# Kernel tuning notes

Hardware: AMD Instinct MI355X
Metric: run time of the kernel (lower is better)

## Reference

```python
import jax, jax.numpy as jnp
import numpy as np
from itertools import combinations_with_replacement

B, T, F, L, POLY_ORDER = 16, 2048, 128, 16, 3


def _hilbert_filter(N):
    # Matches pytorch_hilbert: H[0]=0, H[1:N//2]=2, H[N//2]=0 (even N)
    h = np.zeros(N, dtype=np.float32)
    if N % 2 == 0:
        h[1:N // 2] = 2.0
    else:
        h[1:(N + 1) // 2] = 2.0
    return jnp.asarray(h)


def hilbert(sig, axis=1):
    N = sig.shape[axis]
    Xf = jnp.fft.fft(sig, axis=axis)
    shape = [1] * sig.ndim
    shape[axis] = N
    return jnp.fft.ifft(Xf * _hilbert_filter(N).reshape(shape), axis=axis)


def _combo_indices(latent, poly_order):
    # static index arrays, grouped by degree n
    return [np.array(list(combinations_with_replacement(range(latent), n)), dtype=np.int32)
            for n in range(1, poly_order + 1)]


def compute_library(z, poly_order):
    # z: [B, T, L] -> theta: [B, T, library_dim]
    feats = []
    for combos in _combo_indices(z.shape[-1], poly_order):
        zc = z[..., combos]            # [B, T, ncomb, n]
        feats.append(jnp.prod(zc, axis=-1))  # [B, T, ncomb]
    analytic = hilbert(z, axis=1)
    feats.append(z)
    feats.append(jnp.abs(analytic))    # extract_real_component
    feats.append(jnp.angle(analytic))  # extract_imaginary_component
    return jnp.concatenate(feats, axis=-1)


def setup_inputs() -> dict:
    key = jax.random.key(0)
    ks = jax.random.split(key, 7)
    lib_dim = L + 2 * L + sum(len(c) for c in _combo_indices(L, POLY_ORDER))
    s_enc = 1.0 / np.sqrt(F)
    s_dec = 1.0 / np.sqrt(L)
    s_sin = 1.0 / np.sqrt(lib_dim)
    return {
        "x": jax.random.normal(ks[0], (B, T, F), dtype=jnp.float32),
        "W_enc": jax.random.uniform(ks[1], (L, F), jnp.float32, -s_enc, s_enc),
        "b_enc": jax.random.uniform(ks[2], (L,), jnp.float32, -s_enc, s_enc),
        "W_dec": jax.random.uniform(ks[3], (F, L), jnp.float32, -s_dec, s_dec),
        "b_dec": jax.random.uniform(ks[4], (F,), jnp.float32, -s_dec, s_dec),
        "W_sindy": jax.random.uniform(ks[5], (L, lib_dim), jnp.float32, -s_sin, s_sin),
        "b_sindy": jax.random.uniform(ks[6], (L,), jnp.float32, -s_sin, s_sin),
    }


def reference(x, W_enc, b_enc, W_dec, b_dec, W_sindy, b_sindy):
    z = jnp.einsum('btf,lf->btl', x, W_enc) + b_enc          # encoder
    theta = compute_library(z, POLY_ORDER)                    # [B,T,lib_dim]
    y_hat = jnp.einsum('btd,ld->btl', theta, W_sindy) + b_sindy
    x_hat = jnp.einsum('btl,fl->btf', z, W_dec) + b_dec       # decoder
    # Jacobian of the linear encoder w.r.t. x is the constant weight matrix
    # broadcast per (b, t): identical math to the O((B*T)^2) autograd version.
    jac_z_x = jnp.broadcast_to(W_enc, (x.shape[0], x.shape[1], L, F))
    return (y_hat, x_hat, z, jac_z_x, W_sindy, W_dec)
```

## Files before the change

### kernel.cpp

```cpp
#include <hip/hip_runtime.h>
#include <math.h>

typedef unsigned short u16;
typedef unsigned int   u32;
typedef __attribute__((ext_vector_type(4))) float f32x4;

#define OFF_AT    0
#define OFF_PT    524288
#define OFF_WT    1048576
#define OFF_ZT    1064832
#define OFF_TWC   1589120
#define OFF_TWS   1591168

#define R1_LO 0
#define R1_HI 5592576
#define R2_LO 5592576
#define R2_HI 11185152
#define R3_LO 11185152
#define R3_HI 16777216

__device__ __forceinline__ void jac_range(const float* __restrict__ Wenc,
                                          float* __restrict__ out_jac,
                                          int lo, int hi, int idx, int nth)
{
    const float* wsrc = Wenc + (size_t)((lo + idx) & 511) * 4;
    f32x4 w;
    w.x = wsrc[0]; w.y = wsrc[1]; w.z = wsrc[2]; w.w = wsrc[3];
    f32x4* j4 = (f32x4*)out_jac;
    for (int i = lo + idx; i < hi; i += nth)
        __builtin_nontemporal_store(w, j4 + i);
}

__global__ __launch_bounds__(256) void k1_encdec(
    const float* __restrict__ x, const float* __restrict__ Wenc, const float* __restrict__ benc,
    const float* __restrict__ Wdec, const float* __restrict__ bdec,
    const float* __restrict__ Wsin,
    float* __restrict__ out_z, float* __restrict__ out_xhat,
    float* __restrict__ out_Ws, float* __restrict__ out_Wd,
    float* __restrict__ z_t, float* __restrict__ wt,
    double* __restrict__ twc_g, double* __restrict__ tws_g,
    float* __restrict__ out_jac)
{
    int tid = threadIdx.x;
    int blk = blockIdx.x;

    if (blk >= 1092) {
        jac_range(Wenc, out_jac, R1_LO, R1_HI, (blk - 1092) * 256 + tid, 262144);
        return;
    }
    if (blk >= 1024) {
        int t0 = (blk - 1024) * 256 + tid;
        if (t0 < 16256) {
            float v = Wsin[t0];
            out_Ws[t0] = v;
            int l = t0 / 1016;
            int d = t0 - l * 1016;
            if (d < 16) v += Wsin[t0 + 968];
            wt[d * 16 + l] = v;
        } else if (t0 < 17280) {
            int k = t0 - 16256;
            double ang = -6.283185307179586476925286766559 * (double)k / 2048.0;
            double s_, c_;
            sincos(ang, &s_, &c_);
            twc_g[k] = c_;
            tws_g[k] = s_;
        }
        if (t0 < 2048) out_Wd[t0] = Wdec[t0];
        return;
    }

    __shared__ float xs[32][132];
    __shared__ float we[16][132];
    __shared__ float wdT[16][132];
    __shared__ float zs[32][20];

    {
        const float4* xv = (const float4*)x + (size_t)blk * 1024;
        float4* xs4 = (float4*)&xs[0][0];
        #pragma unroll
        for (int h = 0; h < 4; ++h) {
            int vi = tid + h * 256;
            int pt = vi >> 5, fq = vi & 31;
            xs4[pt * 33 + fq] = xv[vi];
        }
    }
    {
        const float4* wev = (const float4*)Wenc;
        float4* we4 = (float4*)&we[0][0];
        #pragma unroll
        for (int h = 0; h < 2; ++h) {
            int vi = tid + h * 256;
            int l = vi >> 5, fq = vi & 31;
            we4[l * 33 + fq] = wev[vi];
        }
    }
    {
        const float4* wdv = (const float4*)Wdec;
        #pragma unroll
        for (int h = 0; h < 2; ++h) {
            int vi = tid + h * 256;
            float4 v = wdv[vi];
            int f = vi >> 2, lq = (vi & 3) * 4;
            wdT[lq + 0][f] = v.x; wdT[lq + 1][f] = v.y;
            wdT[lq + 2][f] = v.z; wdT[lq + 3][f] = v.w;
        }
    }
    __syncthreads();

    {
        int pt = tid >> 3, lp = tid & 7;
        const float4* xr = (const float4*)&xs[pt][0];
        const float4* wa = (const float4*)&we[lp][0];
        const float4* wb = (const float4*)&we[lp + 8][0];
        float s0 = 0.f, s1 = 0.f;
        #pragma unroll 8
        for (int fq = 0; fq < 32; ++fq) {
            float4 a = xr[fq], u = wa[fq], v = wb[fq];
            s0 = fmaf(a.x, u.x, s0); s0 = fmaf(a.y, u.y, s0);
            s0 = fmaf(a.z, u.z, s0); s0 = fmaf(a.w, u.w, s0);
            s1 = fmaf(a.x, v.x, s1); s1 = fmaf(a.y, v.y, s1);
            s1 = fmaf(a.z, v.z, s1); s1 = fmaf(a.w, v.w, s1);
        }
        zs[pt][lp]     = s0 + benc[lp];
        zs[pt][lp + 8] = s1 + benc[lp + 8];
    }
    __syncthreads();

    {
        #pragma unroll
        for (int h = 0; h < 2; ++h) {
            int i = tid + h * 256;
            out_z[(size_t)blk * 512 + i] = zs[i >> 4][i & 15];
        }
        #pragma unroll
        for (int h = 0; h < 2; ++h) {
            int i = tid + h * 256;
            int l = i >> 5, pt = i & 31;
            z_t[(size_t)l * 32768 + blk * 32 + pt] = zs[pt][l];
        }
    }

    {
        int f = tid & 127, half = tid >> 7;
        float w[16];
        #pragma unroll
        for (int l = 0; l < 16; ++l) w[l] = wdT[l][f];
        float bd = bdec[f];
        #pragma unroll
        for (int p = 0; p < 16; ++p) {
            int pt = half * 16 + p;
            const float4* zr = (const float4*)&zs[pt][0];
            float4 z0 = zr[0], z1 = zr[1], z2 = zr[2], z3 = zr[3];
            float acc = bd;
            acc = fmaf(z0.x, w[0],  acc); acc = fmaf(z0.y, w[1],  acc);
            acc = fmaf(z0.z, w[2],  acc); acc = fmaf(z0.w, w[3],  acc);
            acc = fmaf(z1.x, w[4],  acc); acc = fmaf(z1.y, w[5],  acc);
            acc = fmaf(z1.z, w[6],  acc); acc = fmaf(z1.w, w[7],  acc);
            acc = fmaf(z2.x, w[8],  acc); acc = fmaf(z2.y, w[9],  acc);
            acc = fmaf(z2.z, w[10], acc); acc = fmaf(z2.w, w[11], acc);
            acc = fmaf(z3.x, w[12], acc); acc = fmaf(z3.y, w[13], acc);
            acc = fmaf(z3.z, w[14], acc); acc = fmaf(z3.w, w[15], acc);
            out_xhat[(size_t)blk * 4096 + (size_t)pt * 128 + f] = acc;
        }
    }
}

#define TWPAD(k) ((k) + ((k) >> 5))
#define CP(i)    ((i) + ((i) >> 4))

__global__ __launch_bounds__(1024) void k2_hilbert(
    const float* __restrict__ z_t, const double* __restrict__ twc_g,
    const double* __restrict__ tws_g, const float* __restrict__ Wenc,
    float* __restrict__ a_t, float* __restrict__ p_t,
    float* __restrict__ out_jac)
{
    __shared__ float2 c[2176];
    __shared__ float twc_s[1056];
    __shared__ float tws_s[1056];

    int tid = threadIdx.x;
    if (blockIdx.x >= 256) {
        jac_range(Wenc, out_jac, R2_LO, R2_HI, (blockIdx.x - 256) * 1024 + tid, 524288);
        return;
    }
    int b = blockIdx.x >> 4, l = blockIdx.x & 15;
    const size_t base = (size_t)l * 32768 + (size_t)b * 2048;
    const float* zp = z_t + base;

    {
        twc_s[TWPAD(tid)] = (float)twc_g[tid];
        tws_s[TWPAD(tid)] = (float)tws_g[tid];
    }
    {
        float2 v0; v0.x = zp[tid];        v0.y = 0.0f;
        float2 v1; v1.x = zp[tid + 1024]; v1.y = 0.0f;
        c[CP(tid)] = v0;
        c[CP(tid + 1024)] = v1;
    }
    __syncthreads();

    for (int half = 1024; half >= 1; half >>= 1) {
        int step = 1024 / half;
        int j = tid & (half - 1);
        int pos = ((tid - j) << 1) + j;
        int pa = CP(pos), pb = CP(pos + half);
        int ti = TWPAD(j * step);
        float2 u = c[pa], v = c[pb];
        float wc = twc_s[ti], wsn = tws_s[ti];
        float2 s, dsc;
        s.x = u.x + v.x;  s.y = u.y + v.y;
        float br = u.x - v.x, bi = u.y - v.y;
        dsc.x = br * wc - bi * wsn;
        dsc.y = br * wsn + bi * wc;
        c[pa] = s;
        c[pb] = dsc;
        __syncthreads();
    }

    #pragma unroll
    for (int h = 0; h < 2; ++h) {
        int t = tid + h * 1024;
        float sc = (t == 0 || (t & 1)) ? 0.0f : (2.0f / 2048.0f);
        int ci = CP(t);
        float2 v = c[ci];
        v.x *= sc; v.y *= sc;
        c[ci] = v;
    }
    __syncthreads();

    for (int half = 1; half <= 1024; half <<= 1) {
        int step = 1024 / half;
        int j = tid & (half - 1);
        int pos = ((tid - j) << 1) + j;
        int pa = CP(pos), pb = CP(pos + half);
        int ti = TWPAD(j * step);
        float2 u = c[pa], v = c[pb];
        float wc = twc_s[ti], wsn = tws_s[ti];
        float tr  = v.x * wc + v.y * wsn;
        float ti2 = v.y * wc - v.x * wsn;
        float2 p0, p1;
        p0.x = u.x + tr; p0.y = u.y + ti2;
        p1.x = u.x - tr; p1.y = u.y - ti2;
        c[pa] = p0;
        c[pb] = p1;
        __syncthreads();
    }

    #pragma unroll
    for (int h = 0; h < 2; ++h) {
        int t = tid + h * 1024;
        float2 v = c[CP(t)];
        a_t[base + t] = sqrtf(v.x * v.x + v.y * v.y);
        p_t[base + t] = atan2f(v.y, v.x);
    }
}

#define EMIT2(EXPR) do {                                                    \
    if ((unsigned)(d - LO) < 121u) {                                        \
        float vv[2];                                                        \
        _Pragma("unroll") for (int p = 0; p < 2; ++p) vv[p] = (EXPR);       \
        int bb = (d - LO) << 4;                                             \
        _Pragma("unroll") for (int l = 0; l < 16; ++l) {                    \
            float w = lw[bb + l];                                           \
            acc[0][l] = fmaf(vv[0], w, acc[0][l]);                          \
            acc[1][l] = fmaf(vv[1], w, acc[1][l]);                          \
        }                                                                   \
    }                                                                       \
    ++d;                                                                    \
} while (0)

template<int LO>
__device__ __forceinline__ void poly_accum(const float (&z)[2][16],
                                           const float* __restrict__ lw,
                                           float (&acc)[2][16])
{
    int d = 0;
    #pragma unroll
    for (int i = 0; i < 16; ++i) EMIT2(z[p][i]);
    #pragma unroll
    for (int i = 0; i < 16; ++i)
        #pragma unroll
        for (int j = i; j < 16; ++j) EMIT2(z[p][i] * z[p][j]);
    #pragma unroll
    for (int i = 0; i < 16; ++i)
        #pragma unroll
        for (int j = i; j < 16; ++j)
            #pragma unroll
            for (int k = j; k < 16; ++k) EMIT2(z[p][i] * z[p][j] * z[p][k]);
}

__global__ __launch_bounds__(256, 2) void k3_yhat(
    const float* __restrict__ z_ws, const float* __restrict__ wt,
    const float* __restrict__ Wenc,
    float* __restrict__ part, float* __restrict__ out_jac)
{
    __shared__ float lw[1936];
    int tid = threadIdx.x;
    if (blockIdx.x >= 512) {
        jac_range(Wenc, out_jac, R3_LO, R3_HI, (blockIdx.x - 512) * 256 + tid, 262144);
        return;
    }
    int slice = blockIdx.x >> 6;
    int ptgrp = blockIdx.x & 63;
    int base = ptgrp * 512;

    {
        const float4* src = (const float4*)(wt + slice * 121 * 16);
        float4* dst = (float4*)lw;
        for (int i = tid; i < 484; i += 256) dst[i] = src[i];
    }
    __syncthreads();

    float z[2][16], acc[2][16];
    #pragma unroll
    for (int p = 0; p < 2; ++p) {
        int bt = base + p * 256 + tid;
        const float4* zp = (const float4*)(z_ws + (size_t)bt * 16);
        #pragma unroll
        for (int q = 0; q < 4; ++q) {
            float4 v = zp[q];
            z[p][q*4+0]=v.x; z[p][q*4+1]=v.y; z[p][q*4+2]=v.z; z[p][q*4+3]=v.w;
        }
    }
    #pragma unroll
    for (int p = 0; p < 2; ++p)
        #pragma unroll
        for (int l = 0; l < 16; ++l) acc[p][l] = 0.f;

    switch (slice) {
        case 0: poly_accum<0 * 121>(z, lw, acc); break;
        case 1: poly_accum<1 * 121>(z, lw, acc); break;
        case 2: poly_accum<2 * 121>(z, lw, acc); break;
        case 3: poly_accum<3 * 121>(z, lw, acc); break;
        case 4: poly_accum<4 * 121>(z, lw, acc); break;
        case 5: poly_accum<5 * 121>(z, lw, acc); break;
        case 6: poly_accum<6 * 121>(z, lw, acc); break;
        default: poly_accum<7 * 121>(z, lw, acc); break;
    }

    #pragma unroll
    for (int p = 0; p < 2; ++p) {
        int bt = base + p * 256 + tid;
        float4* pp = (float4*)(part + (size_t)slice * 524288 + (size_t)bt * 16);
        #pragma unroll
        for (int q = 0; q < 4; ++q) {
            float4 v;
            v.x = acc[p][q*4+0]; v.y = acc[p][q*4+1];
            v.z = acc[p][q*4+2]; v.w = acc[p][q*4+3];
            pp[q] = v;
        }
    }
}

__global__ __launch_bounds__(256) void k3_tail(
    const float* __restrict__ part, const float* __restrict__ a_t,
    const float* __restrict__ p_t, const float* __restrict__ wt,
    const float* __restrict__ bsin, float* __restrict__ out_y)
{
    __shared__ float lw[512];
    int tid = threadIdx.x;
    if (tid < 128) {
        ((float4*)lw)[tid] = ((const float4*)(wt + 984 * 16))[tid];
    }
    __syncthreads();

    int bt = blockIdx.x * 128 + (tid >> 1);
    int lh = (tid & 1) * 8;
    float acc[8];
    {
        const float4* bp = (const float4*)bsin;
        #pragma unroll
        for (int q = 0; q < 2; ++q) {
            float4 v = bp[(lh >> 2) + q];
            acc[q*4+0]=v.x; acc[q*4+1]=v.y; acc[q*4+2]=v.z; acc[q*4+3]=v.w;
        }
    }
    #pragma unroll
    for (int sl = 0; sl < 8; ++sl) {
        const float4* pp = (const float4*)(part + (size_t)sl * 524288 + (size_t)bt * 16 + lh);
        #pragma unroll
        for (int q = 0; q < 2; ++q) {
            float4 v = pp[q];
            acc[q*4+0]+=v.x; acc[q*4+1]+=v.y; acc[q*4+2]+=v.z; acc[q*4+3]+=v.w;
        }
    }
    #pragma unroll
    for (int i = 0; i < 16; ++i) {
        float av = a_t[(size_t)i * 32768 + bt];
        #pragma unroll
        for (int l = 0; l < 8; ++l) acc[l] = fmaf(av, lw[i * 16 + lh + l], acc[l]);
    }
    #pragma unroll
    for (int i = 0; i < 16; ++i) {
        float pv = p_t[(size_t)i * 32768 + bt];
        #pragma unroll
        for (int l = 0; l < 8; ++l) acc[l] = fmaf(pv, lw[256 + i * 16 + lh + l], acc[l]);
    }

    float4* yp = (float4*)(out_y + (size_t)bt * 16 + lh);
    #pragma unroll
    for (int q = 0; q < 2; ++q) {
        float4 v;
        v.x = acc[q*4+0]; v.y = acc[q*4+1]; v.z = acc[q*4+2]; v.w = acc[q*4+3];
        yp[q] = v;
    }
}

extern "C" void kernel_launch(void* const* d_in, const int* in_sizes, int n_in,
                              void* d_out, int out_size, void* d_ws, size_t ws_size,
                              hipStream_t stream)
{
    const float* x  = (const float*)d_in[0];
    const float* We = (const float*)d_in[1];
    const float* be = (const float*)d_in[2];
    const float* Wd = (const float*)d_in[3];
    const float* bd = (const float*)d_in[4];
    const float* Ws = (const float*)d_in[5];
    const float* bs = (const float*)d_in[6];

    float* out  = (float*)d_out;
    float* o_y  = out;
    float* o_xh = out + 524288;
    float* o_z  = out + 4718592;
    float* o_j  = out + 5242880;
    float* o_Ws = out + 72351744;
    float* o_Wd = out + 72368000;

    float*  ws    = (float*)d_ws;
    float*  a_t   = ws + OFF_AT;
    float*  p_t   = ws + OFF_PT;
    float*  wt    = ws + OFF_WT;
    float*  z_t   = ws + OFF_ZT;
    double* twc_g = (double*)(ws + OFF_TWC);
    double* tws_g = (double*)(ws + OFF_TWS);
    float*  part  = ws + 1593216;

    hipLaunchKernelGGL(k1_encdec, dim3(2116), dim3(256), 0, stream,
                       x, We, be, Wd, bd, Ws, o_z, o_xh, o_Ws, o_Wd,
                       z_t, wt, twc_g, tws_g, o_j);
    hipLaunchKernelGGL(k2_hilbert, dim3(768), dim3(1024), 0, stream,
                       z_t, twc_g, tws_g, We, a_t, p_t, o_j);
    hipLaunchKernelGGL(k3_yhat, dim3(1536), dim3(256), 0, stream,
                       o_z, wt, We, part, o_j);
    hipLaunchKernelGGL(k3_tail, dim3(256), dim3(256), 0, stream,
                       part, a_t, p_t, wt, bs, o_y);
}
```

Measured before the change: 329.8 us.

## Fuse Hilbert FFT and polynomial y-hat kernels into one launch

Merges the Hilbert-transform FFT kernel and the polynomial library accumulation kernel into a single 256-thread kernel. Block ranges pick FFT work, poly-slice work, or jacobian broadcast stores, and the two jacobian store ranges become one. The FFT is reworked from 1024 threads to 256 threads, each doing four butterflies per stage. This removes a launch boundary so FFT and poly blocks can overlap. In exchange the FFT gets less thread parallelism per block and shares launch bounds and LDS sizing with the poly path.

```diff
diff --git a/kernel.cpp b/kernel.cpp
--- a/kernel.cpp
+++ b/kernel.cpp
@@ -14,10 +14,8 @@
 
 #define R1_LO 0
 #define R1_HI 5592576
-#define R2_LO 5592576
-#define R2_HI 11185152
-#define R3_LO 11185152
-#define R3_HI 16777216
+#define R23_LO 5592576
+#define R23_HI 16777216
 
 __device__ __forceinline__ void jac_range(const float* __restrict__ Wenc,
                                           float* __restrict__ out_jac,
@@ -168,93 +166,6 @@
 #define TWPAD(k) ((k) + ((k) >> 5))
 #define CP(i)    ((i) + ((i) >> 4))
 
-__global__ __launch_bounds__(1024) void k2_hilbert(
-    const float* __restrict__ z_t, const double* __restrict__ twc_g,
-    const double* __restrict__ tws_g, const float* __restrict__ Wenc,
-    float* __restrict__ a_t, float* __restrict__ p_t,
-    float* __restrict__ out_jac)
-{
-    __shared__ float2 c[2176];
-    __shared__ float twc_s[1056];
-    __shared__ float tws_s[1056];
-
-    int tid = threadIdx.x;
-    if (blockIdx.x >= 256) {
-        jac_range(Wenc, out_jac, R2_LO, R2_HI, (blockIdx.x - 256) * 1024 + tid, 524288);
-        return;
-    }
-    int b = blockIdx.x >> 4, l = blockIdx.x & 15;
-    const size_t base = (size_t)l * 32768 + (size_t)b * 2048;
-    const float* zp = z_t + base;
-
-    {
-        twc_s[TWPAD(tid)] = (float)twc_g[tid];
-        tws_s[TWPAD(tid)] = (float)tws_g[tid];
-    }
-    {
-        float2 v0; v0.x = zp[tid];        v0.y = 0.0f;
-        float2 v1; v1.x = zp[tid + 1024]; v1.y = 0.0f;
-        c[CP(tid)] = v0;
-        c[CP(tid + 1024)] = v1;
-    }
-    __syncthreads();
-
-    for (int half = 1024; half >= 1; half >>= 1) {
-        int step = 1024 / half;
-        int j = tid & (half - 1);
-        int pos = ((tid - j) << 1) + j;
-        int pa = CP(pos), pb = CP(pos + half);
-        int ti = TWPAD(j * step);
-        float2 u = c[pa], v = c[pb];
-        float wc = twc_s[ti], wsn = tws_s[ti];
-        float2 s, dsc;
-        s.x = u.x + v.x;  s.y = u.y + v.y;
-        float br = u.x - v.x, bi = u.y - v.y;
-        dsc.x = br * wc - bi * wsn;
-        dsc.y = br * wsn + bi * wc;
-        c[pa] = s;
-        c[pb] = dsc;
-        __syncthreads();
-    }
-
-    #pragma unroll
-    for (int h = 0; h < 2; ++h) {
-        int t = tid + h * 1024;
-        float sc = (t == 0 || (t & 1)) ? 0.0f : (2.0f / 2048.0f);
-        int ci = CP(t);
-        float2 v = c[ci];
-        v.x *= sc; v.y *= sc;
-        c[ci] = v;
-    }
-    __syncthreads();
-
-    for (int half = 1; half <= 1024; half <<= 1) {
-        int step = 1024 / half;
-        int j = tid & (half - 1);
-        int pos = ((tid - j) << 1) + j;
-        int pa = CP(pos), pb = CP(pos + half);
-        int ti = TWPAD(j * step);
-        float2 u = c[pa], v = c[pb];
-        float wc = twc_s[ti], wsn = tws_s[ti];
-        float tr  = v.x * wc + v.y * wsn;
-        float ti2 = v.y * wc - v.x * wsn;
-        float2 p0, p1;
-        p0.x = u.x + tr; p0.y = u.y + ti2;
-        p1.x = u.x - tr; p1.y = u.y - ti2;
-        c[pa] = p0;
-        c[pb] = p1;
-        __syncthreads();
-    }
-
-    #pragma unroll
-    for (int h = 0; h < 2; ++h) {
-        int t = tid + h * 1024;
-        float2 v = c[CP(t)];
-        a_t[base + t] = sqrtf(v.x * v.x + v.y * v.y);
-        p_t[base + t] = atan2f(v.y, v.x);
-    }
-}
-
 #define EMIT2(EXPR) do {                                                    \
     if ((unsigned)(d - LO) < 121u) {                                        \
         float vv[2];                                                        \
@@ -289,65 +200,162 @@
             for (int k = j; k < 16; ++k) EMIT2(z[p][i] * z[p][j] * z[p][k]);
 }
 
-__global__ __launch_bounds__(256, 2) void k3_yhat(
+__global__ __launch_bounds__(256, 2) void k23_fused(
+    const float* __restrict__ z_t, const double* __restrict__ twc_g,
+    const double* __restrict__ tws_g, const float* __restrict__ Wenc,
     const float* __restrict__ z_ws, const float* __restrict__ wt,
-    const float* __restrict__ Wenc,
+    float* __restrict__ a_t, float* __restrict__ p_t,
     float* __restrict__ part, float* __restrict__ out_jac)
 {
-    __shared__ float lw[1936];
+    __shared__ float smem[6464];
     int tid = threadIdx.x;
-    if (blockIdx.x >= 512) {
-        jac_range(Wenc, out_jac, R3_LO, R3_HI, (blockIdx.x - 512) * 256 + tid, 262144);
+    int blk = blockIdx.x;
+
+    if (blk >= 768) {
+        jac_range(Wenc, out_jac, R23_LO, R23_HI, (blk - 768) * 256 + tid, 393216);
         return;
     }
-    int slice = blockIdx.x >> 6;
-    int ptgrp = blockIdx.x & 63;
-    int base = ptgrp * 512;
-
-    {
-        const float4* src = (const float4*)(wt + slice * 121 * 16);
-        float4* dst = (float4*)lw;
-        for (int i = tid; i < 484; i += 256) dst[i] = src[i];
-    }
-    __syncthreads();
-
-    float z[2][16], acc[2][16];
-    #pragma unroll
-    for (int p = 0; p < 2; ++p) {
-        int bt = base + p * 256 + tid;
-        const float4* zp = (const float4*)(z_ws + (size_t)bt * 16);
-        #pragma unroll
-        for (int q = 0; q < 4; ++q) {
-            float4 v = zp[q];
-            z[p][q*4+0]=v.x; z[p][q*4+1]=v.y; z[p][q*4+2]=v.z; z[p][q*4+3]=v.w;
-        }
-    }
-    #pragma unroll
-    for (int p = 0; p < 2; ++p)
-        #pragma unroll
-        for (int l = 0; l < 16; ++l) acc[p][l] = 0.f;
-
-    switch (slice) {
-        case 0: poly_accum<0 * 121>(z, lw, acc); break;
-        case 1: poly_accum<1 * 121>(z, lw, acc); break;
-        case 2: poly_accum<2 * 121>(z, lw, acc); break;
-        case 3: poly_accum<3 * 121>(z, lw, acc); break;
-        case 4: poly_accum<4 * 121>(z, lw, acc); break;
-        case 5: poly_accum<5 * 121>(z, lw, acc); break;
-        case 6: poly_accum<6 * 121>(z, lw, acc); break;
-        default: poly_accum<7 * 121>(z, lw, acc); break;
-    }
-
-    #pragma unroll
-    for (int p = 0; p < 2; ++p) {
-        int bt = base + p * 256 + tid;
-        float4* pp = (float4*)(part + (size_t)slice * 524288 + (size_t)bt * 16);
-        #pragma unroll
-        for (int q = 0; q < 4; ++q) {
-            float4 v;
-            v.x = acc[p][q*4+0]; v.y = acc[p][q*4+1];
-            v.z = acc[p][q*4+2]; v.w = acc[p][q*4+3];
-            pp[q] = v;
+
+    if (blk < 256) {
+        float2* c      = (float2*)smem;
+        float*  twc_s  = smem + 4352;
+        float*  tws_s  = smem + 5408;
+
+        int b = blk >> 4, l = blk & 15;
+        const size_t base = (size_t)l * 32768 + (size_t)b * 2048;
+        const float* zp = z_t + base;
+
+        #pragma unroll
+        for (int h = 0; h < 4; ++h) {
+            int k = tid + h * 256;
+            twc_s[TWPAD(k)] = (float)twc_g[k];
+            tws_s[TWPAD(k)] = (float)tws_g[k];
+        }
+        #pragma unroll
+        for (int h = 0; h < 8; ++h) {
+            int t = tid + h * 256;
+            float2 v; v.x = zp[t]; v.y = 0.0f;
+            c[CP(t)] = v;
+        }
+        __syncthreads();
+
+        for (int half = 1024; half >= 1; half >>= 1) {
+            int step = 1024 / half;
+            #pragma unroll
+            for (int h = 0; h < 4; ++h) {
+                int t = tid + h * 256;
+                int j = t & (half - 1);
+                int pos = ((t - j) << 1) + j;
+                int pa = CP(pos), pb = CP(pos + half);
+                int ti = TWPAD(j * step);
+                float2 u = c[pa], v = c[pb];
+                float wc = twc_s[ti], wsn = tws_s[ti];
+                float2 s, dsc;
+                s.x = u.x + v.x;  s.y = u.y + v.y;
+                float br = u.x - v.x, bi = u.y - v.y;
+                dsc.x = br * wc - bi * wsn;
+                dsc.y = br * wsn + bi * wc;
+                c[pa] = s;
+                c[pb] = dsc;
+            }
+            __syncthreads();
+        }
+
+        #pragma unroll
+        for (int h = 0; h < 8; ++h) {
+            int t = tid + h * 256;
+            float sc = (t == 0 || (t & 1)) ? 0.0f : (2.0f / 2048.0f);
+            int ci = CP(t);
+            float2 v = c[ci];
+            v.x *= sc; v.y *= sc;
+            c[ci] = v;
+        }
+        __syncthreads();
+
+        for (int half = 1; half <= 1024; half <<= 1) {
+            int step = 1024 / half;
+            #pragma unroll
+            for (int h = 0; h < 4; ++h) {
+                int t = tid + h * 256;
+                int j = t & (half - 1);
+                int pos = ((t - j) << 1) + j;
+                int pa = CP(pos), pb = CP(pos + half);
+                int ti = TWPAD(j * step);
+                float2 u = c[pa], v = c[pb];
+                float wc = twc_s[ti], wsn = tws_s[ti];
+                float tr  = v.x * wc + v.y * wsn;
+                float ti2 = v.y * wc - v.x * wsn;
+                float2 p0, p1;
+                p0.x = u.x + tr; p0.y = u.y + ti2;
+                p1.x = u.x - tr; p1.y = u.y - ti2;
+                c[pa] = p0;
+                c[pb] = p1;
+            }
+            __syncthreads();
+        }
+
+        #pragma unroll
+        for (int h = 0; h < 8; ++h) {
+            int t = tid + h * 256;
+            float2 v = c[CP(t)];
+            a_t[base + t] = sqrtf(v.x * v.x + v.y * v.y);
+            p_t[base + t] = atan2f(v.y, v.x);
+        }
+        return;
+    }
+
+    {
+        float* lw = smem;
+        int pb = blk - 256;
+        int slice = pb >> 6;
+        int ptgrp = pb & 63;
+        int base = ptgrp * 512;
+
+        {
+            const float4* src = (const float4*)(wt + slice * 121 * 16);
+            float4* dst = (float4*)lw;
+            for (int i = tid; i < 484; i += 256) dst[i] = src[i];
+        }
+        __syncthreads();
+
+        float z[2][16], acc[2][16];
+        #pragma unroll
+        for (int p = 0; p < 2; ++p) {
+            int bt = base + p * 256 + tid;
+            const float4* zp = (const float4*)(z_ws + (size_t)bt * 16);
+            #pragma unroll
+            for (int q = 0; q < 4; ++q) {
+                float4 v = zp[q];
+                z[p][q*4+0]=v.x; z[p][q*4+1]=v.y; z[p][q*4+2]=v.z; z[p][q*4+3]=v.w;
+            }
+        }
+        #pragma unroll
+        for (int p = 0; p < 2; ++p)
+            #pragma unroll
+            for (int l = 0; l < 16; ++l) acc[p][l] = 0.f;
+
+        switch (slice) {
+            case 0: poly_accum<0 * 121>(z, lw, acc); break;
+            case 1: poly_accum<1 * 121>(z, lw, acc); break;
+            case 2: poly_accum<2 * 121>(z, lw, acc); break;
+            case 3: poly_accum<3 * 121>(z, lw, acc); break;
+            case 4: poly_accum<4 * 121>(z, lw, acc); break;
+            case 5: poly_accum<5 * 121>(z, lw, acc); break;
+            case 6: poly_accum<6 * 121>(z, lw, acc); break;
+            default: poly_accum<7 * 121>(z, lw, acc); break;
+        }
+
+        #pragma unroll
+        for (int p = 0; p < 2; ++p) {
+            int bt = base + p * 256 + tid;
+            float4* pp = (float4*)(part + (size_t)slice * 524288 + (size_t)bt * 16);
+            #pragma unroll
+            for (int q = 0; q < 4; ++q) {
+                float4 v;
+                v.x = acc[p][q*4+0]; v.y = acc[p][q*4+1];
+                v.z = acc[p][q*4+2]; v.w = acc[p][q*4+3];
+                pp[q] = v;
+            }
         }
     }
 }
@@ -438,10 +446,8 @@
     hipLaunchKernelGGL(k1_encdec, dim3(2116), dim3(256), 0, stream,
                        x, We, be, Wd, bd, Ws, o_z, o_xh, o_Ws, o_Wd,
                        z_t, wt, twc_g, tws_g, o_j);
-    hipLaunchKernelGGL(k2_hilbert, dim3(768), dim3(1024), 0, stream,
-                       z_t, twc_g, tws_g, We, a_t, p_t, o_j);
-    hipLaunchKernelGGL(k3_yhat, dim3(1536), dim3(256), 0, stream,
-                       o_z, wt, We, part, o_j);
+    hipLaunchKernelGGL(k23_fused, dim3(2304), dim3(256), 0, stream,
+                       z_t, twc_g, tws_g, We, o_z, wt, a_t, p_t, part, o_j);
     hipLaunchKernelGGL(k3_tail, dim3(256), dim3(256), 0, stream,
                        part, a_t, p_t, wt, bs, o_y);
 }
```

New measurement: 364.9 us. 1.11x slower.
